# Kernel optimization log

Hardware: AMD Instinct MI355X
Metric: run time of the kernel (lower is better)

Reference implementation:

```python
import jax, jax.numpy as jnp
import numpy as np

N = 4096
F_IN = 512
F_OUT = 64
H = 8
ALPHA = 0.2
NEG_BIG = -9e15


def setup_inputs() -> dict:
    key = jax.random.key(0)
    ks = jax.random.split(key, 7)
    h = jax.random.normal(ks[0], (N, F_IN), dtype=jnp.float32)
    mask = jax.random.randint(ks[1], (N, N), 0, 2, dtype=jnp.int32)
    # per-head linear W: weight [H, F_IN, F_OUT], bias [H, F_OUT] (xavier-ish scale)
    w_scale = 1.414 * np.sqrt(6.0 / (F_IN + F_OUT))
    W = jax.random.uniform(ks[2], (H, F_IN, F_OUT), dtype=jnp.float32, minval=-w_scale, maxval=w_scale)
    bW = jnp.zeros((H, F_OUT), dtype=jnp.float32)
    # attention linear A: [2*F_OUT, 1] split into a_l (acts on Wh_i) and a_r (acts on Wh_j)
    a_scale = 1.414 * np.sqrt(6.0 / (2 * F_OUT + 1))
    a_l = jax.random.uniform(ks[3], (H, F_OUT), dtype=jnp.float32, minval=-a_scale, maxval=a_scale)
    a_r = jax.random.uniform(ks[4], (H, F_OUT), dtype=jnp.float32, minval=-a_scale, maxval=a_scale)
    bA = jnp.zeros((H,), dtype=jnp.float32)
    return {"h": h, "mask": mask, "W": W, "bW": bW, "a_l": a_l, "a_r": a_r, "bA": bA}


def reference(h, mask, W, bW, a_l, a_r, bA):
    # Wh: [H, N, F_OUT]
    Wh = jnp.einsum('ni,hio->hno', h, W) + bW[:, None, :]
    # A([Wh_i ; Wh_j]) decomposed as outer sum: e[h,i,j] = a_l.Wh_i + a_r.Wh_j + bA
    el = jnp.einsum('hno,ho->hn', Wh, a_l)  # [H, N]
    er = jnp.einsum('hno,ho->hn', Wh, a_r)  # [H, N]
    e = el[:, :, None] + er[:, None, :] + bA[:, None, None]  # [H, N, N]
    e = jax.nn.leaky_relu(e, negative_slope=ALPHA)
    e = jnp.where(mask[None] > 0, e, NEG_BIG)
    a = jax.nn.softmax(e, axis=-1)  # softmax over neighbors j (dim=1 in torch)
    # dropout omitted (eval mode / deterministic reference)
    aWh = jnp.einsum('hij,hjo->hio', a, Wh)  # [H, N, F_OUT]
    out = jax.nn.elu(aWh)  # last=False
    # concat heads along feature dim -> [N, H*F_OUT]
    return jnp.transpose(out, (1, 0, 2)).reshape(N, H * F_OUT)
```

## Files before the change

### kernel.cpp

```cpp
#include <hip/hip_runtime.h>
#include <hip/hip_bf16.h>

#define NN 4096
#define FIN 512
#define FOUT 64
#define NH 8
#define ALPHA 0.2f

typedef unsigned int uint;
typedef unsigned short ushort;
typedef unsigned char uchar;
typedef __attribute__((ext_vector_type(8))) short short8;
typedef __attribute__((ext_vector_type(4))) float floatx4;

__device__ __forceinline__ float bf2f(ushort s) { return __uint_as_float(((uint)s) << 16); }
__device__ __forceinline__ ushort f2bf(float f) {
    uint u = __float_as_uint(f);
    u += 0x7fffu + ((u >> 16) & 1u);
    return (ushort)(u >> 16);
}
__device__ __forceinline__ short8 u4s8(uint4 v) {
    union { uint4 u; short8 s; } x; x.u = v; return x.s;
}

__global__ void detect_kernel(const ushort* __restrict__ hraw, int* __restrict__ flag) {
    __shared__ int cnt[256];
    int t = threadIdx.x;
    float v = bf2f(hraw[2 * t]);
    float a = fabsf(v);
    cnt[t] = (a >= 1e-3f && a <= 100.0f) ? 1 : 0;
    __syncthreads();
    for (int s = 128; s >= 1; s >>= 1) {
        if (t < s) cnt[t] += cnt[t + s];
        __syncthreads();
    }
    if (t == 0) *flag = (cnt[0] >= 128) ? 1 : 0;
}

#define PM_BLKS 8192
#define CV_BLKS 1024
#define TW_BLKS 32

__global__ __launch_bounds__(256) void prep_kernel(
    const int* __restrict__ mask, uchar* __restrict__ mb,
    const void* __restrict__ hraw, ushort* __restrict__ bh,
    const void* __restrict__ Wraw, ushort* __restrict__ WT,
    const int* __restrict__ flag)
{
    const int b = blockIdx.x, t = threadIdx.x;
    if (b < PM_BLKS) {
        size_t gid = (size_t)b * 256 + t;
        const int* p = mask + gid * 8;
        int4 aa = *(const int4*)p;
        int4 bb = *(const int4*)(p + 4);
        uint by = (uint)(aa.x > 0)        | ((uint)(aa.y > 0) << 1)
                | ((uint)(aa.z > 0) << 2) | ((uint)(aa.w > 0) << 3)
                | ((uint)(bb.x > 0) << 4) | ((uint)(bb.y > 0) << 5)
                | ((uint)(bb.z > 0) << 6) | ((uint)(bb.w > 0) << 7);
        mb[gid] = (uchar)by;
    } else if (b < PM_BLKS + CV_BLKS) {
        size_t e0 = ((size_t)(b - PM_BLKS) * 256 + t) * 8;
        if (*flag) {
            *(uint4*)(bh + e0) = *(const uint4*)((const ushort*)hraw + e0);
        } else {
            const float* s = (const float*)hraw + e0;
            float4 f0 = *(const float4*)s;
            float4 f1 = *(const float4*)(s + 4);
            uint4 o;
            o.x = (uint)f2bf(f0.x) | ((uint)f2bf(f0.y) << 16);
            o.y = (uint)f2bf(f0.z) | ((uint)f2bf(f0.w) << 16);
            o.z = (uint)f2bf(f1.x) | ((uint)f2bf(f1.y) << 16);
            o.w = (uint)f2bf(f1.z) | ((uint)f2bf(f1.w) << 16);
            *(uint4*)(bh + e0) = o;
        }
    } else {
        int b2 = b - PM_BLKS - CV_BLKS;
        int h = b2 >> 2, kq = b2 & 3;
        int o = t & 63, sub = t >> 6;
        int kbase = kq * 128 + sub * 32;
        int isbf = *flag;
        uint pk[16];
#pragma unroll
        for (int kk = 0; kk < 32; kk += 2) {
            float v0, v1;
            size_t s0 = ((size_t)h * FIN + kbase + kk) * FOUT + o;
            size_t s1 = s0 + FOUT;
            if (isbf) { v0 = bf2f(((const ushort*)Wraw)[s0]); v1 = bf2f(((const ushort*)Wraw)[s1]); }
            else      { v0 = ((const float*)Wraw)[s0];        v1 = ((const float*)Wraw)[s1]; }
            pk[kk >> 1] = (uint)f2bf(v0) | ((uint)f2bf(v1) << 16);
        }
        ushort* dst = WT + ((size_t)h * FOUT + o) * FIN + kbase;
#pragma unroll
        for (int q = 0; q < 4; q++)
            *(uint4*)(dst + q * 8) = make_uint4(pk[q*4], pk[q*4+1], pk[q*4+2], pk[q*4+3]);
    }
}

__global__ __launch_bounds__(256) void khv_kernel(const float* __restrict__ er,
                                                  float* __restrict__ Kh,
                                                  float* __restrict__ vt,
                                                  float* __restrict__ zt) {
    __shared__ float red[256];
    int h = blockIdx.x >> 3, sl = blockIdx.x & 7, t = threadIdx.x;
    float m = -3.0e38f;
    for (int j = t; j < NN; j += 256) m = fmaxf(m, er[(size_t)h * NN + j]);
    red[t] = m;
    __syncthreads();
    for (int s = 128; s >= 1; s >>= 1) {
        if (t < s) red[t] = fmaxf(red[t], red[t + s]);
        __syncthreads();
    }
    float kh = red[0];
    if (t == 0 && sl == 0) Kh[h] = kh;
    int j = sl * 512 + t;
#pragma unroll
    for (int q = 0; q < 2; q++, j += 256) {
        float d = er[(size_t)h * NN + j] - kh;
        vt[(size_t)h * NN + j] = __expf(d);
        zt[(size_t)h * NN + j] = __expf(ALPHA * d);
    }
}

__global__ __launch_bounds__(256) void wh_kernel(
    const ushort* __restrict__ hmat, const ushort* __restrict__ WT,
    const void* __restrict__ bWr, const void* __restrict__ alr,
    const void* __restrict__ arr, const void* __restrict__ bAr,
    const int* __restrict__ flag,
    ushort* __restrict__ WhT, float* __restrict__ el, float* __restrict__ er)
{
    __shared__ __align__(16) ushort sT[64][72];
    const int t = threadIdx.x, lane = t & 63, wid = t >> 6;
    const int head = blockIdx.y, rbase = blockIdx.x * 64;
    const int lm = lane & 15, lq = lane >> 4;

    floatx4 C[4];
#pragma unroll
    for (int cg = 0; cg < 4; cg++) C[cg] = (floatx4){0.f, 0.f, 0.f, 0.f};

    const ushort* Ap = hmat + (size_t)(rbase + wid * 16 + lm) * FIN + lq * 8;
    const ushort* Bp = WT + (size_t)head * FOUT * FIN + (size_t)lm * FIN + lq * 8;

#pragma unroll
    for (int kc = 0; kc < 16; kc++) {
        short8 a = *(const short8*)(Ap + kc * 32);
#pragma unroll
        for (int cg = 0; cg < 4; cg++) {
            short8 b = *(const short8*)(Bp + (size_t)cg * 16 * FIN + kc * 32);
            C[cg] = __builtin_amdgcn_mfma_f32_16x16x32_bf16(a, b, C[cg], 0, 0, 0);
        }
    }

    const int isbf = *flag;
    float bA = isbf ? bf2f(((const ushort*)bAr)[head]) : ((const float*)bAr)[head];
    float pel[4] = {0.f, 0.f, 0.f, 0.f}, per[4] = {0.f, 0.f, 0.f, 0.f};
#pragma unroll
    for (int cg = 0; cg < 4; cg++) {
        int o = head * FOUT + cg * 16 + lm;
        float bw = isbf ? bf2f(((const ushort*)bWr)[o]) : ((const float*)bWr)[o];
        float av = isbf ? bf2f(((const ushort*)alr)[o]) : ((const float*)alr)[o];
        float rv = isbf ? bf2f(((const ushort*)arr)[o]) : ((const float*)arr)[o];
        ushort pk[4];
#pragma unroll
        for (int r = 0; r < 4; r++) {
            float v = C[cg][r] + bw;
            pel[r] += v * av;
            per[r] += v * rv;
            pk[r] = f2bf(v);
        }
        ushort4 p4; p4.x = pk[0]; p4.y = pk[1]; p4.z = pk[2]; p4.w = pk[3];
        *(ushort4*)(&sT[cg * 16 + lm][wid * 16 + lq * 4]) = p4;
    }
#pragma unroll
    for (int off = 1; off < 16; off <<= 1) {
#pragma unroll
        for (int r = 0; r < 4; r++) {
            pel[r] += __shfl_xor(pel[r], off);
            per[r] += __shfl_xor(per[r], off);
        }
    }
    if (lm == 0) {
#pragma unroll
        for (int r = 0; r < 4; r++) {
            int row = rbase + wid * 16 + lq * 4 + r;
            el[(size_t)head * NN + row] = pel[r];
            er[(size_t)head * NN + row] = per[r] + bA;
        }
    }
    __syncthreads();
    {
        int o = t >> 2, ch = t & 3;
        uint4 v0 = *(const uint4*)(&sT[o][ch * 16]);
        uint4 v1 = *(const uint4*)(&sT[o][ch * 16 + 8]);
        ushort* d = WhT + ((size_t)head * FOUT + o) * NN + rbase + ch * 16;
        *(uint4*)d = v0;
        *(uint4*)(d + 8) = v1;
    }
}

__device__ __forceinline__ uint ppair(float v0, float v1, float z0, float z1,
                                      uint m2, float ui, float wi, float ti) {
    float p0 = (v0 >= ti) ? ui * v0 : wi * z0;
    float p1 = (v1 >= ti) ? ui * v1 : wi * z1;
    uint k0 = (uint)0 - (m2 & 1u);
    uint k1 = (uint)0 - ((m2 >> 1) & 1u);
    p0 = __uint_as_float(__float_as_uint(p0) & k0);
    p1 = __uint_as_float(__float_as_uint(p1) & k1);
    __hip_bfloat162 r = __float22bfloat162_rn(make_float2(p0, p1));
    return *(uint*)&r;
}

__device__ __forceinline__ short8 pgen8(float4 va, float4 vb, float4 za, float4 zb,
                                        uint mby, float ui, float wi, float ti) {
    union { uint4 u; short8 s; } c;
    c.u.x = ppair(va.x, va.y, za.x, za.y, mby,      ui, wi, ti);
    c.u.y = ppair(va.z, va.w, za.z, za.w, mby >> 2, ui, wi, ti);
    c.u.z = ppair(vb.x, vb.y, zb.x, zb.y, mby >> 4, ui, wi, ti);
    c.u.w = ppair(vb.z, vb.w, zb.z, zb.w, mby >> 6, ui, wi, ti);
    return c.s;
}

__global__ __launch_bounds__(256, 2) void attn_kernel(
    const uchar* __restrict__ mb,
    const ushort* __restrict__ WhT,
    const float* __restrict__ el, const float* __restrict__ Kh,
    const float* __restrict__ vt, const float* __restrict__ zt,
    void* __restrict__ outv, const int* __restrict__ flagp)
{
    __shared__ __align__(16) ushort sB[2][64 * 72];
    __shared__ float sv[2][64];
    __shared__ float sz[2][64];

    const int t = threadIdx.x, lane = t & 63, wid = t >> 6;
    const int b = blockIdx.x;
    const int head = b & 7;
    const int ibase = ((b >> 3) * 4 + wid) * 16;
    const int lm = lane & 15, lq = lane >> 4;
    const int sh8 = lq * 8;

    const float eli = el[(size_t)head * NN + ibase + lm];
    const float kh = Kh[head];
    const float x = eli + kh;
    const float Mi = fmaxf(x, ALPHA * x);
    const float ui = __expf(x - Mi);
    const float wi = __expf(ALPHA * x - Mi);
    const float ti = __expf(-x);

    const int so = t >> 2;
    const int sc = (t & 3) * 16;
    const ushort* gB = WhT + ((size_t)head * FOUT + so) * NN + sc;
    const float* gvt = vt + (size_t)head * NN;
    const float* gzt = zt + (size_t)head * NN;
    const uchar* mrow = mb + (size_t)(ibase + lm) * 512;

    uint4 r0, r1; float rvz = 0.f; uint2 mk_stage;

    auto gload = [&](int j0) {
        r0 = *(const uint4*)(gB + j0);
        r1 = *(const uint4*)(gB + j0 + 8);
        if (t < 128) rvz = (t < 64) ? gvt[j0 + t] : gzt[j0 + t - 64];
        mk_stage = *(const uint2*)(mrow + (j0 >> 3));
    };
    auto lwrite = [&](int buf) {
        *(uint4*)(&sB[buf][so * 72 + sc]) = r0;
        *(uint4*)(&sB[buf][so * 72 + sc + 8]) = r1;
        if (t < 128) { if (t < 64) sv[buf][t] = rvz; else sz[buf][t - 64] = rvz; }
    };

    const short8 ones = {0x3F80, 0x3F80, 0x3F80, 0x3F80, 0x3F80, 0x3F80, 0x3F80, 0x3F80};
    floatx4 C0 = {0.f, 0.f, 0.f, 0.f}, C1 = C0, C2 = C0, C3 = C0, Cd = C0;

    auto compute = [&](int buf, uint2 mk) {
        uint m0 = (mk.x >> sh8) & 0xFFu;
        uint m1 = (mk.y >> sh8) & 0xFFu;
        float4 va = *(const float4*)(&sv[buf][sh8]);
        float4 vb = *(const float4*)(&sv[buf][sh8 + 4]);
        float4 vc = *(const float4*)(&sv[buf][32 + sh8]);
        float4 vd = *(const float4*)(&sv[buf][36 + sh8]);
        float4 za = *(const float4*)(&sz[buf][sh8]);
        float4 zb = *(const float4*)(&sz[buf][sh8 + 4]);
        float4 zc = *(const float4*)(&sz[buf][32 + sh8]);
        float4 zd = *(const float4*)(&sz[buf][36 + sh8]);
        short8 a0 = pgen8(va, vb, za, zb, m0, ui, wi, ti);
        short8 a1 = pgen8(vc, vd, zc, zd, m1, ui, wi, ti);
        const ushort* base = &sB[buf][0];
        short8 b00 = *(const short8*)(base + (0  + lm) * 72 + sh8);
        short8 b10 = *(const short8*)(base + (16 + lm) * 72 + sh8);
        short8 b20 = *(const short8*)(base + (32 + lm) * 72 + sh8);
        short8 b30 = *(const short8*)(base + (48 + lm) * 72 + sh8);
        Cd = __builtin_amdgcn_mfma_f32_16x16x32_bf16(a0, ones, Cd, 0, 0, 0);
        C0 = __builtin_amdgcn_mfma_f32_16x16x32_bf16(a0, b00, C0, 0, 0, 0);
        C1 = __builtin_amdgcn_mfma_f32_16x16x32_bf16(a0, b10, C1, 0, 0, 0);
        C2 = __builtin_amdgcn_mfma_f32_16x16x32_bf16(a0, b20, C2, 0, 0, 0);
        C3 = __builtin_amdgcn_mfma_f32_16x16x32_bf16(a0, b30, C3, 0, 0, 0);
        short8 b01 = *(const short8*)(base + (0  + lm) * 72 + 32 + sh8);
        short8 b11 = *(const short8*)(base + (16 + lm) * 72 + 32 + sh8);
        short8 b21 = *(const short8*)(base + (32 + lm) * 72 + 32 + sh8);
        short8 b31 = *(const short8*)(base + (48 + lm) * 72 + 32 + sh8);
        Cd = __builtin_amdgcn_mfma_f32_16x16x32_bf16(a1, ones, Cd, 0, 0, 0);
        C0 = __builtin_amdgcn_mfma_f32_16x16x32_bf16(a1, b01, C0, 0, 0, 0);
        C1 = __builtin_amdgcn_mfma_f32_16x16x32_bf16(a1, b11, C1, 0, 0, 0);
        C2 = __builtin_amdgcn_mfma_f32_16x16x32_bf16(a1, b21, C2, 0, 0, 0);
        C3 = __builtin_amdgcn_mfma_f32_16x16x32_bf16(a1, b31, C3, 0, 0, 0);
    };

    gload(0);
    lwrite(0);
    uint2 mk0 = mk_stage;
    gload(64);
    __syncthreads();

    for (int it = 0; it < 64; it++) {
        compute(it & 1, mk0);
        if (it < 63) {
            __syncthreads();
            lwrite((it + 1) & 1);
            mk0 = mk_stage;
            gload(((it + 2) & 63) * 64);
            __syncthreads();
        }
    }

    const int isbf = *flagp;
#pragma unroll
    for (int r = 0; r < 4; r++) {
        int row = ibase + lq * 4 + r;
        float inv = 1.f / Cd[r];
        float x0 = C0[r] * inv; x0 = (x0 > 0.f) ? x0 : __expf(x0) - 1.f;
        float x1 = C1[r] * inv; x1 = (x1 > 0.f) ? x1 : __expf(x1) - 1.f;
        float x2 = C2[r] * inv; x2 = (x2 > 0.f) ? x2 : __expf(x2) - 1.f;
        float x3 = C3[r] * inv; x3 = (x3 > 0.f) ? x3 : __expf(x3) - 1.f;
        size_t base = (size_t)row * (NH * FOUT) + head * FOUT + lm;
        if (isbf) {
            ushort* o = (ushort*)outv;
            o[base + 0]  = f2bf(x0);
            o[base + 16] = f2bf(x1);
            o[base + 32] = f2bf(x2);
            o[base + 48] = f2bf(x3);
        } else {
            float* o = (float*)outv;
            o[base + 0]  = x0;
            o[base + 16] = x1;
            o[base + 32] = x2;
            o[base + 48] = x3;
        }
    }
}

extern "C" void kernel_launch(void* const* d_in, const int* in_sizes, int n_in,
                              void* d_out, int out_size, void* d_ws, size_t ws_size,
                              hipStream_t stream)
{
    const void* hraw = d_in[0];
    const int*  mask = (const int*)d_in[1];
    const void* Wraw = d_in[2];
    const void* bWr  = d_in[3];
    const void* alr  = d_in[4];
    const void* arr  = d_in[5];
    const void* bAr  = d_in[6];

    char* w = (char*)d_ws;
    int*    flag = (int*)w;                     w += 16;
    ushort* bh   = (ushort*)w;                  w += (size_t)NN * FIN * 2;
    ushort* WT   = (ushort*)w;                  w += (size_t)NH * FOUT * FIN * 2;
    ushort* WhT  = (ushort*)w;                  w += (size_t)NH * FOUT * NN * 2;
    float*  el   = (float*)w;                   w += (size_t)NH * NN * 4;
    float*  er   = (float*)w;                   w += (size_t)NH * NN * 4;
    float*  Kh   = (float*)w;                   w += 64;
    float*  vt   = (float*)w;                   w += (size_t)NH * NN * 4;
    float*  zt   = (float*)w;                   w += (size_t)NH * NN * 4;
    uchar*  mb   = (uchar*)w;                   w += (size_t)NN * 512;

    detect_kernel<<<1, 256, 0, stream>>>((const ushort*)hraw, flag);
    prep_kernel<<<PM_BLKS + CV_BLKS + TW_BLKS, 256, 0, stream>>>(
        mask, mb, hraw, bh, Wraw, WT, flag);
    wh_kernel<<<dim3(NN / 64, NH), 256, 0, stream>>>(bh, WT, bWr, alr, arr, bAr, flag,
                                                     WhT, el, er);
    khv_kernel<<<64, 256, 0, stream>>>(er, Kh, vt, zt);
    attn_kernel<<<NN / 64 * NH, 256, 0, stream>>>(mb, WhT, el, Kh, vt, zt, d_out, flag);
}
```

Measured before the change: 196.0 us.

## Fuse dtype detection and column-softmax prep into consumers; widen attention rows per wave

```diff
diff --git a/kernel.cpp b/kernel.cpp
--- a/kernel.cpp
+++ b/kernel.cpp
@@ -10,6 +10,7 @@
 typedef unsigned int uint;
 typedef unsigned short ushort;
 typedef unsigned char uchar;
+typedef unsigned long long ull;
 typedef __attribute__((ext_vector_type(8))) short short8;
 typedef __attribute__((ext_vector_type(4))) float floatx4;
 
@@ -19,22 +20,12 @@
     u += 0x7fffu + ((u >> 16) & 1u);
     return (ushort)(u >> 16);
 }
-__device__ __forceinline__ short8 u4s8(uint4 v) {
-    union { uint4 u; short8 s; } x; x.u = v; return x.s;
-}
-
-__global__ void detect_kernel(const ushort* __restrict__ hraw, int* __restrict__ flag) {
-    __shared__ int cnt[256];
-    int t = threadIdx.x;
-    float v = bf2f(hraw[2 * t]);
-    float a = fabsf(v);
-    cnt[t] = (a >= 1e-3f && a <= 100.0f) ? 1 : 0;
-    __syncthreads();
-    for (int s = 128; s >= 1; s >>= 1) {
-        if (t < s) cnt[t] += cnt[t + s];
-        __syncthreads();
-    }
-    if (t == 0) *flag = (cnt[0] >= 128) ? 1 : 0;
+
+__device__ __forceinline__ int detect_bf16(const ushort* __restrict__ hraw) {
+    int lane = threadIdx.x & 63;
+    float a = fabsf(bf2f(hraw[2 * lane]));
+    ull bal = __ballot(a >= 1e-3f && a <= 100.0f);
+    return __popcll(bal) >= 32;
 }
 
 #define PM_BLKS 8192
@@ -44,8 +35,7 @@
 __global__ __launch_bounds__(256) void prep_kernel(
     const int* __restrict__ mask, uchar* __restrict__ mb,
     const void* __restrict__ hraw, ushort* __restrict__ bh,
-    const void* __restrict__ Wraw, ushort* __restrict__ WT,
-    const int* __restrict__ flag)
+    const void* __restrict__ Wraw, ushort* __restrict__ WT)
 {
     const int b = blockIdx.x, t = threadIdx.x;
     if (b < PM_BLKS) {
@@ -59,8 +49,9 @@
                 | ((uint)(bb.z > 0) << 6) | ((uint)(bb.w > 0) << 7);
         mb[gid] = (uchar)by;
     } else if (b < PM_BLKS + CV_BLKS) {
+        int isbf = detect_bf16((const ushort*)hraw);
         size_t e0 = ((size_t)(b - PM_BLKS) * 256 + t) * 8;
-        if (*flag) {
+        if (isbf) {
             *(uint4*)(bh + e0) = *(const uint4*)((const ushort*)hraw + e0);
         } else {
             const float* s = (const float*)hraw + e0;
@@ -74,11 +65,11 @@
             *(uint4*)(bh + e0) = o;
         }
     } else {
+        int isbf = detect_bf16((const ushort*)hraw);
         int b2 = b - PM_BLKS - CV_BLKS;
         int h = b2 >> 2, kq = b2 & 3;
         int o = t & 63, sub = t >> 6;
         int kbase = kq * 128 + sub * 32;
-        int isbf = *flag;
         uint pk[16];
 #pragma unroll
         for (int kk = 0; kk < 32; kk += 2) {
@@ -96,36 +87,11 @@
     }
 }
 
-__global__ __launch_bounds__(256) void khv_kernel(const float* __restrict__ er,
-                                                  float* __restrict__ Kh,
-                                                  float* __restrict__ vt,
-                                                  float* __restrict__ zt) {
-    __shared__ float red[256];
-    int h = blockIdx.x >> 3, sl = blockIdx.x & 7, t = threadIdx.x;
-    float m = -3.0e38f;
-    for (int j = t; j < NN; j += 256) m = fmaxf(m, er[(size_t)h * NN + j]);
-    red[t] = m;
-    __syncthreads();
-    for (int s = 128; s >= 1; s >>= 1) {
-        if (t < s) red[t] = fmaxf(red[t], red[t + s]);
-        __syncthreads();
-    }
-    float kh = red[0];
-    if (t == 0 && sl == 0) Kh[h] = kh;
-    int j = sl * 512 + t;
-#pragma unroll
-    for (int q = 0; q < 2; q++, j += 256) {
-        float d = er[(size_t)h * NN + j] - kh;
-        vt[(size_t)h * NN + j] = __expf(d);
-        zt[(size_t)h * NN + j] = __expf(ALPHA * d);
-    }
-}
-
 __global__ __launch_bounds__(256) void wh_kernel(
     const ushort* __restrict__ hmat, const ushort* __restrict__ WT,
     const void* __restrict__ bWr, const void* __restrict__ alr,
     const void* __restrict__ arr, const void* __restrict__ bAr,
-    const int* __restrict__ flag,
+    const ushort* __restrict__ hraw,
     ushort* __restrict__ WhT, float* __restrict__ el, float* __restrict__ er)
 {
     __shared__ __align__(16) ushort sT[64][72];
@@ -150,7 +116,7 @@
         }
     }
 
-    const int isbf = *flag;
+    const int isbf = detect_bf16(hraw);
     float bA = isbf ? bf2f(((const ushort*)bAr)[head]) : ((const float*)bAr)[head];
     float pel[4] = {0.f, 0.f, 0.f, 0.f}, per[4] = {0.f, 0.f, 0.f, 0.f};
 #pragma unroll
@@ -219,129 +185,163 @@
     return c.s;
 }
 
-__global__ __launch_bounds__(256, 2) void attn_kernel(
+__global__ __launch_bounds__(128) void attn_kernel(
     const uchar* __restrict__ mb,
     const ushort* __restrict__ WhT,
-    const float* __restrict__ el, const float* __restrict__ Kh,
-    const float* __restrict__ vt, const float* __restrict__ zt,
-    void* __restrict__ outv, const int* __restrict__ flagp)
+    const float* __restrict__ el, const float* __restrict__ er,
+    const ushort* __restrict__ hraw,
+    void* __restrict__ outv)
 {
     __shared__ __align__(16) ushort sB[2][64 * 72];
-    __shared__ float sv[2][64];
-    __shared__ float sz[2][64];
+    __shared__ __align__(16) float sV[NN];
+    __shared__ __align__(16) float sZ[NN];
+    __shared__ float sRed[2];
 
     const int t = threadIdx.x, lane = t & 63, wid = t >> 6;
     const int b = blockIdx.x;
     const int head = b & 7;
-    const int ibase = ((b >> 3) * 4 + wid) * 16;
-    const int lm = lane & 15, lq = lane >> 4;
-    const int sh8 = lq * 8;
-
-    const float eli = el[(size_t)head * NN + ibase + lm];
-    const float kh = Kh[head];
-    const float x = eli + kh;
-    const float Mi = fmaxf(x, ALPHA * x);
-    const float ui = __expf(x - Mi);
-    const float wi = __expf(ALPHA * x - Mi);
-    const float ti = __expf(-x);
-
-    const int so = t >> 2;
-    const int sc = (t & 3) * 16;
+    const int ibase = (b >> 3) * 64;
+    const int lm = lane & 15, lq = lane >> 4, sh8 = lq * 8;
+    const int isbf = detect_bf16(hraw);
+
+    const float* erh = er + (size_t)head * NN;
+    float mx = -3.0e38f;
+    for (int j = t; j < NN; j += 128) mx = fmaxf(mx, erh[j]);
+#pragma unroll
+    for (int off = 32; off >= 1; off >>= 1) mx = fmaxf(mx, __shfl_xor(mx, off));
+    if (lane == 0) sRed[wid] = mx;
+    __syncthreads();
+    const float kh = fmaxf(sRed[0], sRed[1]);
+    for (int j = t; j < NN; j += 128) {
+        float d = erh[j] - kh;
+        sV[j] = __expf(d);
+        sZ[j] = __expf(ALPHA * d);
+    }
+
+    const int row0 = ibase + wid * 32 + lm;
+    float x0 = el[(size_t)head * NN + row0] + kh;
+    float x1 = el[(size_t)head * NN + row0 + 16] + kh;
+    float Mi0 = fmaxf(x0, ALPHA * x0), Mi1 = fmaxf(x1, ALPHA * x1);
+    float ui0 = __expf(x0 - Mi0), wi0 = __expf(ALPHA * x0 - Mi0), ti0 = __expf(-x0);
+    float ui1 = __expf(x1 - Mi1), wi1 = __expf(ALPHA * x1 - Mi1), ti1 = __expf(-x1);
+
+    const uchar* mrow0 = mb + (size_t)row0 * 512;
+    const uchar* mrow1 = mb + (size_t)(row0 + 16) * 512;
+
+    const int so = t >> 1, sc = (t & 1) * 32;
     const ushort* gB = WhT + ((size_t)head * FOUT + so) * NN + sc;
-    const float* gvt = vt + (size_t)head * NN;
-    const float* gzt = zt + (size_t)head * NN;
-    const uchar* mrow = mb + (size_t)(ibase + lm) * 512;
-
-    uint4 r0, r1; float rvz = 0.f; uint2 mk_stage;
+    uint4 rB[4]; uint2 mkS0, mkS1;
 
     auto gload = [&](int j0) {
-        r0 = *(const uint4*)(gB + j0);
-        r1 = *(const uint4*)(gB + j0 + 8);
-        if (t < 128) rvz = (t < 64) ? gvt[j0 + t] : gzt[j0 + t - 64];
-        mk_stage = *(const uint2*)(mrow + (j0 >> 3));
+#pragma unroll
+        for (int q = 0; q < 4; q++) rB[q] = *(const uint4*)(gB + j0 + q * 8);
+        mkS0 = *(const uint2*)(mrow0 + (j0 >> 3));
+        mkS1 = *(const uint2*)(mrow1 + (j0 >> 3));
     };
     auto lwrite = [&](int buf) {
-        *(uint4*)(&sB[buf][so * 72 + sc]) = r0;
-        *(uint4*)(&sB[buf][so * 72 + sc + 8]) = r1;
-        if (t < 128) { if (t < 64) sv[buf][t] = rvz; else sz[buf][t - 64] = rvz; }
+#pragma unroll
+        for (int q = 0; q < 4; q++)
+            *(uint4*)(&sB[buf][so * 72 + sc + q * 8]) = rB[q];
     };
 
     const short8 ones = {0x3F80, 0x3F80, 0x3F80, 0x3F80, 0x3F80, 0x3F80, 0x3F80, 0x3F80};
-    floatx4 C0 = {0.f, 0.f, 0.f, 0.f}, C1 = C0, C2 = C0, C3 = C0, Cd = C0;
-
-    auto compute = [&](int buf, uint2 mk) {
-        uint m0 = (mk.x >> sh8) & 0xFFu;
-        uint m1 = (mk.y >> sh8) & 0xFFu;
-        float4 va = *(const float4*)(&sv[buf][sh8]);
-        float4 vb = *(const float4*)(&sv[buf][sh8 + 4]);
-        float4 vc = *(const float4*)(&sv[buf][32 + sh8]);
-        float4 vd = *(const float4*)(&sv[buf][36 + sh8]);
-        float4 za = *(const float4*)(&sz[buf][sh8]);
-        float4 zb = *(const float4*)(&sz[buf][sh8 + 4]);
-        float4 zc = *(const float4*)(&sz[buf][32 + sh8]);
-        float4 zd = *(const float4*)(&sz[buf][36 + sh8]);
-        short8 a0 = pgen8(va, vb, za, zb, m0, ui, wi, ti);
-        short8 a1 = pgen8(vc, vd, zc, zd, m1, ui, wi, ti);
+    floatx4 C[2][4], Cd[2];
+#pragma unroll
+    for (int s = 0; s < 2; s++) {
+        Cd[s] = (floatx4){0.f, 0.f, 0.f, 0.f};
+#pragma unroll
+        for (int g = 0; g < 4; g++) C[s][g] = (floatx4){0.f, 0.f, 0.f, 0.f};
+    }
+
+    auto compute = [&](int buf, int j0, uint2 mk0, uint2 mk1) {
+        float4 va = *(const float4*)(&sV[j0 + sh8]);
+        float4 vb = *(const float4*)(&sV[j0 + sh8 + 4]);
+        float4 vc = *(const float4*)(&sV[j0 + 32 + sh8]);
+        float4 vd = *(const float4*)(&sV[j0 + 32 + sh8 + 4]);
+        float4 za = *(const float4*)(&sZ[j0 + sh8]);
+        float4 zb = *(const float4*)(&sZ[j0 + sh8 + 4]);
+        float4 zc = *(const float4*)(&sZ[j0 + 32 + sh8]);
+        float4 zd = *(const float4*)(&sZ[j0 + 32 + sh8 + 4]);
+        short8 a00 = pgen8(va, vb, za, zb, (mk0.x >> sh8) & 0xFFu, ui0, wi0, ti0);
+        short8 a01 = pgen8(vc, vd, zc, zd, (mk0.y >> sh8) & 0xFFu, ui0, wi0, ti0);
+        short8 a10 = pgen8(va, vb, za, zb, (mk1.x >> sh8) & 0xFFu, ui1, wi1, ti1);
+        short8 a11 = pgen8(vc, vd, zc, zd, (mk1.y >> sh8) & 0xFFu, ui1, wi1, ti1);
         const ushort* base = &sB[buf][0];
-        short8 b00 = *(const short8*)(base + (0  + lm) * 72 + sh8);
-        short8 b10 = *(const short8*)(base + (16 + lm) * 72 + sh8);
-        short8 b20 = *(const short8*)(base + (32 + lm) * 72 + sh8);
-        short8 b30 = *(const short8*)(base + (48 + lm) * 72 + sh8);
-        Cd = __builtin_amdgcn_mfma_f32_16x16x32_bf16(a0, ones, Cd, 0, 0, 0);
-        C0 = __builtin_amdgcn_mfma_f32_16x16x32_bf16(a0, b00, C0, 0, 0, 0);
-        C1 = __builtin_amdgcn_mfma_f32_16x16x32_bf16(a0, b10, C1, 0, 0, 0);
-        C2 = __builtin_amdgcn_mfma_f32_16x16x32_bf16(a0, b20, C2, 0, 0, 0);
-        C3 = __builtin_amdgcn_mfma_f32_16x16x32_bf16(a0, b30, C3, 0, 0, 0);
-        short8 b01 = *(const short8*)(base + (0  + lm) * 72 + 32 + sh8);
-        short8 b11 = *(const short8*)(base + (16 + lm) * 72 + 32 + sh8);
-        short8 b21 = *(const short8*)(base + (32 + lm) * 72 + 32 + sh8);
-        short8 b31 = *(const short8*)(base + (48 + lm) * 72 + 32 + sh8);
-        Cd = __builtin_amdgcn_mfma_f32_16x16x32_bf16(a1, ones, Cd, 0, 0, 0);
-        C0 = __builtin_amdgcn_mfma_f32_16x16x32_bf16(a1, b01, C0, 0, 0, 0);
-        C1 = __builtin_amdgcn_mfma_f32_16x16x32_bf16(a1, b11, C1, 0, 0, 0);
-        C2 = __builtin_amdgcn_mfma_f32_16x16x32_bf16(a1, b21, C2, 0, 0, 0);
-        C3 = __builtin_amdgcn_mfma_f32_16x16x32_bf16(a1, b31, C3, 0, 0, 0);
+        {
+            short8 b0 = *(const short8*)(base + (0  + lm) * 72 + sh8);
+            short8 b1 = *(const short8*)(base + (16 + lm) * 72 + sh8);
+            short8 b2 = *(const short8*)(base + (32 + lm) * 72 + sh8);
+            short8 b3 = *(const short8*)(base + (48 + lm) * 72 + sh8);
+            Cd[0] = __builtin_amdgcn_mfma_f32_16x16x32_bf16(a00, ones, Cd[0], 0, 0, 0);
+            Cd[1] = __builtin_amdgcn_mfma_f32_16x16x32_bf16(a10, ones, Cd[1], 0, 0, 0);
+            C[0][0] = __builtin_amdgcn_mfma_f32_16x16x32_bf16(a00, b0, C[0][0], 0, 0, 0);
+            C[1][0] = __builtin_amdgcn_mfma_f32_16x16x32_bf16(a10, b0, C[1][0], 0, 0, 0);
+            C[0][1] = __builtin_amdgcn_mfma_f32_16x16x32_bf16(a00, b1, C[0][1], 0, 0, 0);
+            C[1][1] = __builtin_amdgcn_mfma_f32_16x16x32_bf16(a10, b1, C[1][1], 0, 0, 0);
+            C[0][2] = __builtin_amdgcn_mfma_f32_16x16x32_bf16(a00, b2, C[0][2], 0, 0, 0);
+            C[1][2] = __builtin_amdgcn_mfma_f32_16x16x32_bf16(a10, b2, C[1][2], 0, 0, 0);
+            C[0][3] = __builtin_amdgcn_mfma_f32_16x16x32_bf16(a00, b3, C[0][3], 0, 0, 0);
+            C[1][3] = __builtin_amdgcn_mfma_f32_16x16x32_bf16(a10, b3, C[1][3], 0, 0, 0);
+        }
+        {
+            short8 b0 = *(const short8*)(base + (0  + lm) * 72 + 32 + sh8);
+            short8 b1 = *(const short8*)(base + (16 + lm) * 72 + 32 + sh8);
+            short8 b2 = *(const short8*)(base + (32 + lm) * 72 + 32 + sh8);
+            short8 b3 = *(const short8*)(base + (48 + lm) * 72 + 32 + sh8);
+            Cd[0] = __builtin_amdgcn_mfma_f32_16x16x32_bf16(a01, ones, Cd[0], 0, 0, 0);
+            Cd[1] = __builtin_amdgcn_mfma_f32_16x16x32_bf16(a11, ones, Cd[1], 0, 0, 0);
+            C[0][0] = __builtin_amdgcn_mfma_f32_16x16x32_bf16(a01, b0, C[0][0], 0, 0, 0);
+            C[1][0] = __builtin_amdgcn_mfma_f32_16x16x32_bf16(a11, b0, C[1][0], 0, 0, 0);
+            C[0][1] = __builtin_amdgcn_mfma_f32_16x16x32_bf16(a01, b1, C[0][1], 0, 0, 0);
+            C[1][1] = __builtin_amdgcn_mfma_f32_16x16x32_bf16(a11, b1, C[1][1], 0, 0, 0);
+            C[0][2] = __builtin_amdgcn_mfma_f32_16x16x32_bf16(a01, b2, C[0][2], 0, 0, 0);
+            C[1][2] = __builtin_amdgcn_mfma_f32_16x16x32_bf16(a11, b2, C[1][2], 0, 0, 0);
+            C[0][3] = __builtin_amdgcn_mfma_f32_16x16x32_bf16(a01, b3, C[0][3], 0, 0, 0);
+            C[1][3] = __builtin_amdgcn_mfma_f32_16x16x32_bf16(a11, b3, C[1][3], 0, 0, 0);
+        }
     };
 
     gload(0);
     lwrite(0);
-    uint2 mk0 = mk_stage;
+    uint2 mk0 = mkS0, mk1 = mkS1;
     gload(64);
     __syncthreads();
 
     for (int it = 0; it < 64; it++) {
-        compute(it & 1, mk0);
+        compute(it & 1, it * 64, mk0, mk1);
         if (it < 63) {
             __syncthreads();
             lwrite((it + 1) & 1);
-            mk0 = mk_stage;
+            mk0 = mkS0; mk1 = mkS1;
             gload(((it + 2) & 63) * 64);
             __syncthreads();
         }
     }
 
-    const int isbf = *flagp;
-#pragma unroll
-    for (int r = 0; r < 4; r++) {
-        int row = ibase + lq * 4 + r;
-        float inv = 1.f / Cd[r];
-        float x0 = C0[r] * inv; x0 = (x0 > 0.f) ? x0 : __expf(x0) - 1.f;
-        float x1 = C1[r] * inv; x1 = (x1 > 0.f) ? x1 : __expf(x1) - 1.f;
-        float x2 = C2[r] * inv; x2 = (x2 > 0.f) ? x2 : __expf(x2) - 1.f;
-        float x3 = C3[r] * inv; x3 = (x3 > 0.f) ? x3 : __expf(x3) - 1.f;
-        size_t base = (size_t)row * (NH * FOUT) + head * FOUT + lm;
-        if (isbf) {
-            ushort* o = (ushort*)outv;
-            o[base + 0]  = f2bf(x0);
-            o[base + 16] = f2bf(x1);
-            o[base + 32] = f2bf(x2);
-            o[base + 48] = f2bf(x3);
-        } else {
-            float* o = (float*)outv;
-            o[base + 0]  = x0;
-            o[base + 16] = x1;
-            o[base + 32] = x2;
-            o[base + 48] = x3;
+#pragma unroll
+    for (int s = 0; s < 2; s++) {
+#pragma unroll
+        for (int r = 0; r < 4; r++) {
+            int row = ibase + wid * 32 + s * 16 + lq * 4 + r;
+            float inv = 1.f / Cd[s][r];
+            float x0e = C[s][0][r] * inv; x0e = (x0e > 0.f) ? x0e : __expf(x0e) - 1.f;
+            float x1e = C[s][1][r] * inv; x1e = (x1e > 0.f) ? x1e : __expf(x1e) - 1.f;
+            float x2e = C[s][2][r] * inv; x2e = (x2e > 0.f) ? x2e : __expf(x2e) - 1.f;
+            float x3e = C[s][3][r] * inv; x3e = (x3e > 0.f) ? x3e : __expf(x3e) - 1.f;
+            size_t base = (size_t)row * (NH * FOUT) + head * FOUT + lm;
+            if (isbf) {
+                ushort* o = (ushort*)outv;
+                o[base + 0]  = f2bf(x0e);
+                o[base + 16] = f2bf(x1e);
+                o[base + 32] = f2bf(x2e);
+                o[base + 48] = f2bf(x3e);
+            } else {
+                float* o = (float*)outv;
+                o[base + 0]  = x0e;
+                o[base + 16] = x1e;
+                o[base + 32] = x2e;
+                o[base + 48] = x3e;
+            }
         }
     }
 }
@@ -359,22 +359,17 @@
     const void* bAr  = d_in[6];
 
     char* w = (char*)d_ws;
-    int*    flag = (int*)w;                     w += 16;
     ushort* bh   = (ushort*)w;                  w += (size_t)NN * FIN * 2;
     ushort* WT   = (ushort*)w;                  w += (size_t)NH * FOUT * FIN * 2;
     ushort* WhT  = (ushort*)w;                  w += (size_t)NH * FOUT * NN * 2;
     float*  el   = (float*)w;                   w += (size_t)NH * NN * 4;
     float*  er   = (float*)w;                   w += (size_t)NH * NN * 4;
-    float*  Kh   = (float*)w;                   w += 64;
-    float*  vt   = (float*)w;                   w += (size_t)NH * NN * 4;
-    float*  zt   = (float*)w;                   w += (size_t)NH * NN * 4;
     uchar*  mb   = (uchar*)w;                   w += (size_t)NN * 512;
 
-    detect_kernel<<<1, 256, 0, stream>>>((const ushort*)hraw, flag);
     prep_kernel<<<PM_BLKS + CV_BLKS + TW_BLKS, 256, 0, stream>>>(
-        mask, mb, hraw, bh, Wraw, WT, flag);
-    wh_kernel<<<dim3(NN / 64, NH), 256, 0, stream>>>(bh, WT, bWr, alr, arr, bAr, flag,
-                                                     WhT, el, er);
-    khv_kernel<<<64, 256, 0, stream>>>(er, Kh, vt, zt);
-    attn_kernel<<<NN / 64 * NH, 256, 0, stream>>>(mb, WhT, el, Kh, vt, zt, d_out, flag);
-}
+        mask, mb, hraw, bh, Wraw, WT);
+    wh_kernel<<<dim3(NN / 64, NH), 256, 0, stream>>>(bh, WT, bWr, alr, arr, bAr,
+                                                     (const ushort*)hraw, WhT, el, er);
+    attn_kernel<<<NN / 64 * NH, 128, 0, stream>>>(mb, WhT, el, er,
+                                                  (const ushort*)hraw, d_out);
+}
```

Result: slower. 230.5 us (+17.6%).

## Inline dtype detection per wave and shrink attention blocks to two waves

Applied to the files above, without the earlier changes.

```diff
diff --git a/kernel.cpp b/kernel.cpp
--- a/kernel.cpp
+++ b/kernel.cpp
@@ -10,6 +10,7 @@
 typedef unsigned int uint;
 typedef unsigned short ushort;
 typedef unsigned char uchar;
+typedef unsigned long long ull;
 typedef __attribute__((ext_vector_type(8))) short short8;
 typedef __attribute__((ext_vector_type(4))) float floatx4;
 
@@ -19,22 +20,12 @@
     u += 0x7fffu + ((u >> 16) & 1u);
     return (ushort)(u >> 16);
 }
-__device__ __forceinline__ short8 u4s8(uint4 v) {
-    union { uint4 u; short8 s; } x; x.u = v; return x.s;
-}
-
-__global__ void detect_kernel(const ushort* __restrict__ hraw, int* __restrict__ flag) {
-    __shared__ int cnt[256];
-    int t = threadIdx.x;
-    float v = bf2f(hraw[2 * t]);
-    float a = fabsf(v);
-    cnt[t] = (a >= 1e-3f && a <= 100.0f) ? 1 : 0;
-    __syncthreads();
-    for (int s = 128; s >= 1; s >>= 1) {
-        if (t < s) cnt[t] += cnt[t + s];
-        __syncthreads();
-    }
-    if (t == 0) *flag = (cnt[0] >= 128) ? 1 : 0;
+
+__device__ __forceinline__ int detect_bf16(const ushort* __restrict__ hraw) {
+    int lane = threadIdx.x & 63;
+    float a = fabsf(bf2f(hraw[2 * lane]));
+    ull bal = __ballot(a >= 1e-3f && a <= 100.0f);
+    return __popcll(bal) >= 32;
 }
 
 #define PM_BLKS 8192
@@ -44,8 +35,7 @@
 __global__ __launch_bounds__(256) void prep_kernel(
     const int* __restrict__ mask, uchar* __restrict__ mb,
     const void* __restrict__ hraw, ushort* __restrict__ bh,
-    const void* __restrict__ Wraw, ushort* __restrict__ WT,
-    const int* __restrict__ flag)
+    const void* __restrict__ Wraw, ushort* __restrict__ WT)
 {
     const int b = blockIdx.x, t = threadIdx.x;
     if (b < PM_BLKS) {
@@ -59,8 +49,9 @@
                 | ((uint)(bb.z > 0) << 6) | ((uint)(bb.w > 0) << 7);
         mb[gid] = (uchar)by;
     } else if (b < PM_BLKS + CV_BLKS) {
+        int isbf = detect_bf16((const ushort*)hraw);
         size_t e0 = ((size_t)(b - PM_BLKS) * 256 + t) * 8;
-        if (*flag) {
+        if (isbf) {
             *(uint4*)(bh + e0) = *(const uint4*)((const ushort*)hraw + e0);
         } else {
             const float* s = (const float*)hraw + e0;
@@ -74,11 +65,11 @@
             *(uint4*)(bh + e0) = o;
         }
     } else {
+        int isbf = detect_bf16((const ushort*)hraw);
         int b2 = b - PM_BLKS - CV_BLKS;
         int h = b2 >> 2, kq = b2 & 3;
         int o = t & 63, sub = t >> 6;
         int kbase = kq * 128 + sub * 32;
-        int isbf = *flag;
         uint pk[16];
 #pragma unroll
         for (int kk = 0; kk < 32; kk += 2) {
@@ -125,7 +116,7 @@
     const ushort* __restrict__ hmat, const ushort* __restrict__ WT,
     const void* __restrict__ bWr, const void* __restrict__ alr,
     const void* __restrict__ arr, const void* __restrict__ bAr,
-    const int* __restrict__ flag,
+    const ushort* __restrict__ hraw,
     ushort* __restrict__ WhT, float* __restrict__ el, float* __restrict__ er)
 {
     __shared__ __align__(16) ushort sT[64][72];
@@ -150,7 +141,7 @@
         }
     }
 
-    const int isbf = *flag;
+    const int isbf = detect_bf16(hraw);
     float bA = isbf ? bf2f(((const ushort*)bAr)[head]) : ((const float*)bAr)[head];
     float pel[4] = {0.f, 0.f, 0.f, 0.f}, per[4] = {0.f, 0.f, 0.f, 0.f};
 #pragma unroll
@@ -219,67 +210,63 @@
     return c.s;
 }
 
-__global__ __launch_bounds__(256, 2) void attn_kernel(
+__global__ __launch_bounds__(128, 2) void attn_kernel(
     const uchar* __restrict__ mb,
     const ushort* __restrict__ WhT,
     const float* __restrict__ el, const float* __restrict__ Kh,
     const float* __restrict__ vt, const float* __restrict__ zt,
-    void* __restrict__ outv, const int* __restrict__ flagp)
+    const ushort* __restrict__ hraw,
+    void* __restrict__ outv)
 {
     __shared__ __align__(16) ushort sB[2][64 * 72];
-    __shared__ float sv[2][64];
-    __shared__ float sz[2][64];
 
     const int t = threadIdx.x, lane = t & 63, wid = t >> 6;
     const int b = blockIdx.x;
     const int head = b & 7;
-    const int ibase = ((b >> 3) * 4 + wid) * 16;
-    const int lm = lane & 15, lq = lane >> 4;
-    const int sh8 = lq * 8;
-
-    const float eli = el[(size_t)head * NN + ibase + lm];
+    const int ibase = (b >> 3) * 32;
+    const int lm = lane & 15, lq = lane >> 4, sh8 = lq * 8;
+
     const float kh = Kh[head];
-    const float x = eli + kh;
+    const int myrow = ibase + wid * 16 + lm;
+    const float x = el[(size_t)head * NN + myrow] + kh;
     const float Mi = fmaxf(x, ALPHA * x);
     const float ui = __expf(x - Mi);
     const float wi = __expf(ALPHA * x - Mi);
     const float ti = __expf(-x);
 
-    const int so = t >> 2;
-    const int sc = (t & 3) * 16;
+    const float* vp = vt + (size_t)head * NN;
+    const float* zp = zt + (size_t)head * NN;
+    const uchar* mrow = mb + (size_t)myrow * 512;
+
+    const int so = t >> 1, sc = (t & 1) * 32;
     const ushort* gB = WhT + ((size_t)head * FOUT + so) * NN + sc;
-    const float* gvt = vt + (size_t)head * NN;
-    const float* gzt = zt + (size_t)head * NN;
-    const uchar* mrow = mb + (size_t)(ibase + lm) * 512;
-
-    uint4 r0, r1; float rvz = 0.f; uint2 mk_stage;
+    uint4 rB[4]; uint2 mkS;
 
     auto gload = [&](int j0) {
-        r0 = *(const uint4*)(gB + j0);
-        r1 = *(const uint4*)(gB + j0 + 8);
-        if (t < 128) rvz = (t < 64) ? gvt[j0 + t] : gzt[j0 + t - 64];
-        mk_stage = *(const uint2*)(mrow + (j0 >> 3));
+#pragma unroll
+        for (int q = 0; q < 4; q++) rB[q] = *(const uint4*)(gB + j0 + q * 8);
+        mkS = *(const uint2*)(mrow + (j0 >> 3));
     };
     auto lwrite = [&](int buf) {
-        *(uint4*)(&sB[buf][so * 72 + sc]) = r0;
-        *(uint4*)(&sB[buf][so * 72 + sc + 8]) = r1;
-        if (t < 128) { if (t < 64) sv[buf][t] = rvz; else sz[buf][t - 64] = rvz; }
+#pragma unroll
+        for (int q = 0; q < 4; q++)
+            *(uint4*)(&sB[buf][so * 72 + sc + q * 8]) = rB[q];
     };
 
     const short8 ones = {0x3F80, 0x3F80, 0x3F80, 0x3F80, 0x3F80, 0x3F80, 0x3F80, 0x3F80};
     floatx4 C0 = {0.f, 0.f, 0.f, 0.f}, C1 = C0, C2 = C0, C3 = C0, Cd = C0;
 
-    auto compute = [&](int buf, uint2 mk) {
+    auto compute = [&](int buf, int j0, uint2 mk) {
         uint m0 = (mk.x >> sh8) & 0xFFu;
         uint m1 = (mk.y >> sh8) & 0xFFu;
-        float4 va = *(const float4*)(&sv[buf][sh8]);
-        float4 vb = *(const float4*)(&sv[buf][sh8 + 4]);
-        float4 vc = *(const float4*)(&sv[buf][32 + sh8]);
-        float4 vd = *(const float4*)(&sv[buf][36 + sh8]);
-        float4 za = *(const float4*)(&sz[buf][sh8]);
-        float4 zb = *(const float4*)(&sz[buf][sh8 + 4]);
-        float4 zc = *(const float4*)(&sz[buf][32 + sh8]);
-        float4 zd = *(const float4*)(&sz[buf][36 + sh8]);
+        float4 va = *(const float4*)(vp + j0 + sh8);
+        float4 vb = *(const float4*)(vp + j0 + sh8 + 4);
+        float4 vc = *(const float4*)(vp + j0 + 32 + sh8);
+        float4 vd = *(const float4*)(vp + j0 + 32 + sh8 + 4);
+        float4 za = *(const float4*)(zp + j0 + sh8);
+        float4 zb = *(const float4*)(zp + j0 + sh8 + 4);
+        float4 zc = *(const float4*)(zp + j0 + 32 + sh8);
+        float4 zd = *(const float4*)(zp + j0 + 32 + sh8 + 4);
         short8 a0 = pgen8(va, vb, za, zb, m0, ui, wi, ti);
         short8 a1 = pgen8(vc, vd, zc, zd, m1, ui, wi, ti);
         const ushort* base = &sB[buf][0];
@@ -305,25 +292,25 @@
 
     gload(0);
     lwrite(0);
-    uint2 mk0 = mk_stage;
+    uint2 mk0 = mkS;
     gload(64);
     __syncthreads();
 
     for (int it = 0; it < 64; it++) {
-        compute(it & 1, mk0);
+        compute(it & 1, it * 64, mk0);
         if (it < 63) {
             __syncthreads();
             lwrite((it + 1) & 1);
-            mk0 = mk_stage;
+            mk0 = mkS;
             gload(((it + 2) & 63) * 64);
             __syncthreads();
         }
     }
 
-    const int isbf = *flagp;
+    const int isbf = detect_bf16(hraw);
 #pragma unroll
     for (int r = 0; r < 4; r++) {
-        int row = ibase + lq * 4 + r;
+        int row = ibase + wid * 16 + lq * 4 + r;
         float inv = 1.f / Cd[r];
         float x0 = C0[r] * inv; x0 = (x0 > 0.f) ? x0 : __expf(x0) - 1.f;
         float x1 = C1[r] * inv; x1 = (x1 > 0.f) ? x1 : __expf(x1) - 1.f;
@@ -359,7 +346,6 @@
     const void* bAr  = d_in[6];
 
     char* w = (char*)d_ws;
-    int*    flag = (int*)w;                     w += 16;
     ushort* bh   = (ushort*)w;                  w += (size_t)NN * FIN * 2;
     ushort* WT   = (ushort*)w;                  w += (size_t)NH * FOUT * FIN * 2;
     ushort* WhT  = (ushort*)w;                  w += (size_t)NH * FOUT * NN * 2;
@@ -370,11 +356,11 @@
     float*  zt   = (float*)w;                   w += (size_t)NH * NN * 4;
     uchar*  mb   = (uchar*)w;                   w += (size_t)NN * 512;
 
-    detect_kernel<<<1, 256, 0, stream>>>((const ushort*)hraw, flag);
     prep_kernel<<<PM_BLKS + CV_BLKS + TW_BLKS, 256, 0, stream>>>(
-        mask, mb, hraw, bh, Wraw, WT, flag);
-    wh_kernel<<<dim3(NN / 64, NH), 256, 0, stream>>>(bh, WT, bWr, alr, arr, bAr, flag,
-                                                     WhT, el, er);
+        mask, mb, hraw, bh, Wraw, WT);
+    wh_kernel<<<dim3(NN / 64, NH), 256, 0, stream>>>(bh, WT, bWr, alr, arr, bAr,
+                                                     (const ushort*)hraw, WhT, el, er);
     khv_kernel<<<64, 256, 0, stream>>>(er, Kh, vt, zt);
-    attn_kernel<<<NN / 64 * NH, 256, 0, stream>>>(mb, WhT, el, Kh, vt, zt, d_out, flag);
-}
+    attn_kernel<<<NN / 32 * NH, 128, 0, stream>>>(mb, WhT, el, Kh, vt, zt,
+                                                  (const ushort*)hraw, d_out);
+}
```

Result: slower. 306.6 us (+56.5%).
